# Kernel tuning notes

Hardware: AMD Instinct MI355X
Metric: run time of the kernel (lower is better)

Reference implementation:

```python
import jax, jax.numpy as jnp
import numpy as np
import math

DIM_MODEL = 1024
N_HEAD = 16
NUM_NEURON = 64
MAX_LEN = 2048
B, S = 4, 2048


def setup_inputs() -> dict:
    key = jax.random.key(0)
    ks = jax.random.split(key, 11)
    d, p = DIM_MODEL, N_HEAD * NUM_NEURON
    sc_in = 1.0 / math.sqrt(d)
    sc_p = 1.0 / math.sqrt(p)
    return {
        "q": jax.random.normal(ks[0], (B, S, d), jnp.float32),
        "k": jax.random.normal(ks[1], (B, S, d), jnp.float32),
        "v": jax.random.normal(ks[2], (B, S, d), jnp.float32),
        "Wq": jax.random.normal(ks[3], (d, p), jnp.float32) * sc_in,
        "bq": jnp.zeros((p,), jnp.float32),
        "Wk": jax.random.normal(ks[4], (d, p), jnp.float32) * sc_in,
        "bk": jnp.zeros((p,), jnp.float32),
        "Wv": jax.random.normal(ks[5], (d, p), jnp.float32) * sc_in,
        "bv": jnp.zeros((p,), jnp.float32),
        "Wf": jax.random.normal(ks[6], (p, d), jnp.float32) * sc_p,
        "bf": jnp.zeros((d,), jnp.float32),
    }


def _split_heads(x):  # [B,S,H*Dh] -> [B,H,S,Dh]
    b, s, _ = x.shape
    return x.reshape(b, s, N_HEAD, NUM_NEURON).transpose(0, 2, 1, 3)


def reference(q, k, v, Wq, bq, Wk, bk, Wv, bv, Wf, bf):
    qh = _split_heads(q @ Wq + bq)
    kh = _split_heads(k @ Wk + bk)
    vh = _split_heads(v @ Wv + bv)
    # NOTE: original scales by 1/sqrt(max_len), not 1/sqrt(head_dim)
    scores = jnp.einsum("bhqd,bhkd->bhqk", qh, kh) / math.sqrt(MAX_LEN)
    s = scores.shape[-1]
    causal = jnp.tril(jnp.ones((s, s), bool))  # [S,S]
    scores = jnp.where(causal[None, None], scores, -jnp.inf)
    attn = jax.nn.softmax(scores, axis=-1)
    out = jnp.einsum("bhqk,bhkd->bhqd", attn, vh)  # [B,H,S,Dh]
    c = out.transpose(0, 2, 1, 3).reshape(out.shape[0], out.shape[2], N_HEAD * NUM_NEURON)
    return c @ Wf + bf
```

## Files before the change

kernel.cpp:

```cpp
#include <hip/hip_runtime.h>
#include <stdint.h>

#define DMODEL 1024
#define NHEAD 16
#define DH 64
#define BB 4
#define SS 2048
#define MROWS (BB * SS)

typedef __bf16 bfx8 __attribute__((ext_vector_type(8)));
typedef float f32x4 __attribute__((ext_vector_type(4)));
typedef float fvec4 __attribute__((ext_vector_type(4)));
typedef int i32x4 __attribute__((ext_vector_type(4)));
typedef unsigned short u16x8 __attribute__((ext_vector_type(8)));
typedef unsigned short u16x4 __attribute__((ext_vector_type(4)));

__device__ __forceinline__ unsigned short f2bf(float f) {
    union { float f; unsigned int u; } v; v.f = f;
    unsigned int r = v.u + 0x7FFFu + ((v.u >> 16) & 1u);
    return (unsigned short)(r >> 16);
}

__device__ __forceinline__ unsigned int cvtpk(float lo, float hi) {
    unsigned int r;
    asm("v_cvt_pk_bf16_f32 %0, %1, %2" : "=v"(r) : "v"(lo), "v"(hi));
    return r;
}

typedef __attribute__((address_space(1))) const void gas_t;
typedef __attribute__((address_space(3))) void las_t;
__device__ __forceinline__ void gload_lds16(const void* g, void* l) {
    __builtin_amdgcn_global_load_lds((gas_t*)g, (las_t*)l, 16, 0, 0);
}

__device__ __forceinline__ int sigma_k(int i) {
    return (i & 0x20) | ((i & 0x0C) << 1) | ((i & 0x10) >> 2) | (i & 3);
}

__global__ void cvt3_kernel(const float* __restrict__ s0, const float* __restrict__ s1,
                            const float* __restrict__ s2,
                            unsigned short* __restrict__ d0, unsigned short* __restrict__ d1,
                            unsigned short* __restrict__ d2, int n8)
{
    const float* s = (blockIdx.y == 0) ? s0 : (blockIdx.y == 1) ? s1 : s2;
    unsigned short* d = (blockIdx.y == 0) ? d0 : (blockIdx.y == 1) ? d1 : d2;
    int i = blockIdx.x * blockDim.x + threadIdx.x;
    if (i >= n8) return;
    fvec4 a = *reinterpret_cast<const fvec4*>(&s[(size_t)i * 8]);
    fvec4 b = *reinterpret_cast<const fvec4*>(&s[(size_t)i * 8 + 4]);
    u16x8 o;
    #pragma unroll
    for (int j = 0; j < 4; ++j) { o[j] = f2bf(a[j]); o[j + 4] = f2bf(b[j]); }
    *reinterpret_cast<u16x8*>(&d[(size_t)i * 8]) = o;
}

__global__ void transpose_cvt3_kernel(const float* __restrict__ W0, unsigned short* __restrict__ T0,
                                      const float* __restrict__ W1, unsigned short* __restrict__ T1,
                                      const float* __restrict__ W2, unsigned short* __restrict__ T2)
{
    const float* W = (blockIdx.z == 0) ? W0 : (blockIdx.z == 1) ? W1 : W2;
    unsigned short* Wt = (blockIdx.z == 0) ? T0 : (blockIdx.z == 1) ? T1 : T2;
    __shared__ unsigned short t[64][72];
    const int tid = threadIdx.x;
    const int r0 = blockIdx.y * 64, c0 = blockIdx.x * 64;
    #pragma unroll
    for (int i = 0; i < 4; ++i) {
        int idx = tid + i * 256;
        int r = idx >> 4, c4 = idx & 15;
        fvec4 v = *reinterpret_cast<const fvec4*>(&W[(size_t)(r0 + r) * DMODEL + c0 + c4 * 4]);
        #pragma unroll
        for (int j = 0; j < 4; ++j) t[c4 * 4 + j][r] = f2bf(v[j]);
    }
    __syncthreads();
    #pragma unroll
    for (int i = 0; i < 2; ++i) {
        int idx = tid + i * 256;
        int r = idx >> 3, c8 = idx & 7;
        u16x8 v = *reinterpret_cast<const u16x8*>(&t[r][c8 * 8]);
        *reinterpret_cast<u16x8*>(&Wt[(size_t)(c0 + r) * DMODEL + r0 + c8 * 8]) = v;
    }
}

struct GArg {
    const unsigned short* A;
    const unsigned short* Bt;
    const float* bias;
    void* O;
    float osc;
    int mode;
};

__global__ __launch_bounds__(256, 2)
void gemm_kernel(GArg g0, GArg g1, int M, int N, int K)
{
    const GArg g = blockIdx.z ? g1 : g0;
    __shared__ unsigned short sA[128 * 64];
    __shared__ unsigned short sB[128 * 64];
    const int tid  = threadIdx.x;
    const int lane = tid & 63;
    const int wave = tid >> 6;
    const int wm = (wave >> 1) * 64, wn = (wave & 1) * 64;
    const int m0 = blockIdx.x * 128, n0 = blockIdx.y * 128;
    const int lr = lane & 15;
    const int lg = lane >> 4;

    f32x4 acc[4][4] = {};

    for (int kk0 = 0; kk0 < K; kk0 += 64) {
        __syncthreads();
        #pragma unroll
        for (int i = 0; i < 4; ++i) {
            int c = tid + i * 256;
            int row = c >> 3, col8 = c & 7;
            gload_lds16(&g.A[(size_t)(m0 + row) * K + kk0 + col8 * 8], &sA[c * 8]);
        }
        #pragma unroll
        for (int i = 0; i < 4; ++i) {
            int c = tid + i * 256;
            int row = c >> 3, col8 = c & 7;
            gload_lds16(&g.Bt[(size_t)(n0 + row) * K + kk0 + col8 * 8], &sB[c * 8]);
        }
        __syncthreads();

        bfx8 af[4][2], bfr[4][2];
        #pragma unroll
        for (int m = 0; m < 4; ++m)
            #pragma unroll
            for (int kk = 0; kk < 2; ++kk)
                af[m][kk] = *reinterpret_cast<const bfx8*>(
                    &sA[(wm + m * 16 + lr) * 64 + kk * 32 + lg * 8]);
        #pragma unroll
        for (int n = 0; n < 4; ++n)
            #pragma unroll
            for (int kk = 0; kk < 2; ++kk)
                bfr[n][kk] = *reinterpret_cast<const bfx8*>(
                    &sB[(wn + n * 16 + lr) * 64 + kk * 32 + lg * 8]);
        #pragma unroll
        for (int kk = 0; kk < 2; ++kk)
            #pragma unroll
            for (int m = 0; m < 4; ++m)
                #pragma unroll
                for (int n = 0; n < 4; ++n)
                    acc[m][n] = __builtin_amdgcn_mfma_f32_16x16x32_bf16(
                        af[m][kk], bfr[n][kk], acc[m][n], 0, 0, 0);
    }

    #pragma unroll
    for (int n = 0; n < 4; ++n) {
        int col = n0 + wn + n * 16 + lr;
        float bv = g.bias[col];
        #pragma unroll
        for (int m = 0; m < 4; ++m) {
            int rowb = m0 + wm + m * 16 + lg * 4;
            float val[4];
            #pragma unroll
            for (int r = 0; r < 4; ++r) val[r] = (acc[m][n][r] + bv) * g.osc;
            if (g.mode == 0) {
                #pragma unroll
                for (int r = 0; r < 4; ++r)
                    ((unsigned short*)g.O)[(size_t)(rowb + r) * N + col] = f2bf(val[r]);
            } else if (g.mode == 2) {
                #pragma unroll
                for (int r = 0; r < 4; ++r)
                    ((float*)g.O)[(size_t)(rowb + r) * N + col] = val[r];
            } else {
                int bq = rowb >> 11, s = rowb & 2047;
                int hh = col >> 6, d = col & 63;
                u16x4 pk;
                #pragma unroll
                for (int r = 0; r < 4; ++r) pk[r] = f2bf(val[r]);
                size_t idx = ((size_t)(bq * 16 + hh) * 64 + d) * 2048 + s;
                *reinterpret_cast<u16x4*>(&((unsigned short*)g.O)[idx]) = pk;
            }
        }
    }
}

__global__ __launch_bounds__(256, 2)
void attn_kernel(const unsigned short* __restrict__ Q,
                 const unsigned short* __restrict__ K,
                 const unsigned short* __restrict__ Vt,
                 unsigned short* __restrict__ C)
{
    __shared__ unsigned short sK[64 * 64];
    __shared__ unsigned short sV[64 * 64];

    const int tid  = threadIdx.x;
    const int lane = tid & 63;
    const int wave = tid >> 6;
    const int lr = lane & 15, lg = lane >> 4;
    const int bh = blockIdx.x;
    const int qt = (int)(gridDim.y - 1) - (int)blockIdx.y;
    const int b = bh >> 4, h = bh & 15;
    const int q0 = qt * 128;
    const size_t rowbase = (size_t)b * SS;
    const int hcol = h * DH;

    const int srow = tid >> 3, sc8 = tid & 7;
    const int sig0 = sigma_k(srow), sig1 = sigma_k(srow + 32);
    const int woff0 = srow * 64 + ((sc8 ^ (srow & 7)) * 8);
    const int woff1 = (srow + 32) * 64 + ((sc8 ^ (srow & 7)) * 8);
    const int p0 = lg ^ (lr & 7);

    bfx8 aq[2][2];
    #pragma unroll
    for (int m = 0; m < 2; ++m) {
        int qr = q0 + wave * 32 + m * 16 + lr;
        const unsigned short* p = &Q[(rowbase + qr) * DMODEL + hcol + lg * 8];
        aq[m][0] = *reinterpret_cast<const bfx8*>(p);
        aq[m][1] = *reinterpret_cast<const bfx8*>(p + 32);
    }

    float m_run[2] = {0.f, 0.f};
    f32x4 l4[2] = {};
    f32x4 acc_o[2][4] = {};
    bool mz = true;
    const int qmax_wave = q0 + wave * 32 + 31;
    const int ntiles = 2 * qt + 2;

    u16x8 rk0, rk1, rv0, rv1;
    {
        rk0 = *reinterpret_cast<const u16x8*>(&K[(rowbase + 0 + sig0) * DMODEL + hcol + sc8 * 8]);
        rk1 = *reinterpret_cast<const u16x8*>(&K[(rowbase + 0 + sig1) * DMODEL + hcol + sc8 * 8]);
        rv0 = *reinterpret_cast<const u16x8*>(&Vt[((size_t)bh * DH + srow) * SS + 0 + sc8 * 8]);
        rv1 = *reinterpret_cast<const u16x8*>(&Vt[((size_t)bh * DH + srow + 32) * SS + 0 + sc8 * 8]);
    }

    for (int t = 0; t < ntiles; ++t) {
        __syncthreads();
        *reinterpret_cast<u16x8*>(&sK[woff0]) = rk0;
        *reinterpret_cast<u16x8*>(&sK[woff1]) = rk1;
        *reinterpret_cast<u16x8*>(&sV[woff0]) = rv0;
        *reinterpret_cast<u16x8*>(&sV[woff1]) = rv1;
        __syncthreads();
        if (t + 1 < ntiles) {
            const int kk = (t + 1) * 64;
            rk0 = *reinterpret_cast<const u16x8*>(&K[(rowbase + kk + sig0) * DMODEL + hcol + sc8 * 8]);
            rk1 = *reinterpret_cast<const u16x8*>(&K[(rowbase + kk + sig1) * DMODEL + hcol + sc8 * 8]);
            rv0 = *reinterpret_cast<const u16x8*>(&Vt[((size_t)bh * DH + srow) * SS + kk + sc8 * 8]);
            rv1 = *reinterpret_cast<const u16x8*>(&Vt[((size_t)bh * DH + srow + 32) * SS + kk + sc8 * 8]);
        }
        const int k0 = t * 64;
        if (k0 > qmax_wave) continue;

        f32x4 sc[2][4];
        __builtin_amdgcn_s_setprio(1);
        #pragma unroll
        for (int nf = 0; nf < 4; ++nf) {
            int i = nf * 16 + lr;
            bfx8 ak0 = *reinterpret_cast<const bfx8*>(&sK[i * 64 + p0 * 8]);
            bfx8 ak1 = *reinterpret_cast<const bfx8*>(&sK[i * 64 + (p0 ^ 4) * 8]);
            #pragma unroll
            for (int m = 0; m < 2; ++m) {
                f32x4 s = {0.f, 0.f, 0.f, 0.f};
                s = __builtin_amdgcn_mfma_f32_16x16x32_bf16(ak0, aq[m][0], s, 0, 0, 0);
                s = __builtin_amdgcn_mfma_f32_16x16x32_bf16(ak1, aq[m][1], s, 0, 0, 0);
                sc[m][nf] = s;
            }
        }
        __builtin_amdgcn_s_setprio(0);
        #pragma unroll
        for (int m = 0; m < 2; ++m) {
            if (k0 + 63 > q0 + wave * 32 + m * 16) {
                int qrow = q0 + wave * 32 + m * 16 + lr;
                #pragma unroll
                for (int nf = 0; nf < 4; ++nf) {
                    int kb = k0 + ((nf >> 1) << 5) + (lg << 3) + ((nf & 1) << 2);
                    #pragma unroll
                    for (int r = 0; r < 4; ++r)
                        if (kb + r > qrow) sc[m][nf][r] = -3.0e38f;
                }
            }
        }
        f32x4 mx4 = sc[0][0];
        #pragma unroll
        for (int m = 0; m < 2; ++m)
            #pragma unroll
            for (int nf = 0; nf < 4; ++nf)
                #pragma unroll
                for (int r = 0; r < 4; ++r) mx4[r] = fmaxf(mx4[r], sc[m][nf][r]);
        float pmax = fmaxf(fmaxf(mx4[0], mx4[1]), fmaxf(mx4[2], mx4[3]));
        if (mz && __all(pmax <= 8.0f)) {
            #pragma unroll
            for (int m = 0; m < 2; ++m)
                #pragma unroll
                for (int nf = 0; nf < 4; ++nf) {
                    #pragma unroll
                    for (int r = 0; r < 4; ++r)
                        sc[m][nf][r] = __builtin_exp2f(sc[m][nf][r]);
                    l4[m] += sc[m][nf];
                }
        } else {
            mz = false;
            #pragma unroll
            for (int m = 0; m < 2; ++m) {
                float mx = -3.0e38f;
                #pragma unroll
                for (int nf = 0; nf < 4; ++nf)
                    #pragma unroll
                    for (int r = 0; r < 4; ++r) mx = fmaxf(mx, sc[m][nf][r]);
                mx = fmaxf(mx, __shfl_xor(mx, 16, 64));
                mx = fmaxf(mx, __shfl_xor(mx, 32, 64));
                float mnew = fmaxf(m_run[m], mx);
                float fs = __builtin_exp2f(m_run[m] - mnew);
                m_run[m] = mnew;
                f32x4 ps = {0.f, 0.f, 0.f, 0.f};
                #pragma unroll
                for (int nf = 0; nf < 4; ++nf) {
                    #pragma unroll
                    for (int r = 0; r < 4; ++r)
                        sc[m][nf][r] = __builtin_exp2f(sc[m][nf][r] - mnew);
                    ps += sc[m][nf];
                }
                #pragma unroll
                for (int r = 0; r < 4; ++r) l4[m][r] = l4[m][r] * fs + ps[r];
                #pragma unroll
                for (int r = 0; r < 4; ++r) {
                    float fsa = __shfl(fs, lg * 4 + r, 64);
                    #pragma unroll
                    for (int d = 0; d < 4; ++d) acc_o[m][d][r] *= fsa;
                }
            }
        }
        #pragma unroll
        for (int h2 = 0; h2 < 2; ++h2) {
            union { i32x4 i; bfx8 b; } pa[2];
            #pragma unroll
            for (int m = 0; m < 2; ++m) {
                pa[m].i[0] = cvtpk(sc[m][2 * h2][0],     sc[m][2 * h2][1]);
                pa[m].i[1] = cvtpk(sc[m][2 * h2][2],     sc[m][2 * h2][3]);
                pa[m].i[2] = cvtpk(sc[m][2 * h2 + 1][0], sc[m][2 * h2 + 1][1]);
                pa[m].i[3] = cvtpk(sc[m][2 * h2 + 1][2], sc[m][2 * h2 + 1][3]);
            }
            __builtin_amdgcn_s_setprio(1);
            #pragma unroll
            for (int d = 0; d < 4; ++d) {
                int i = d * 16 + lr;
                int pv = ((h2 << 2) | lg) ^ (lr & 7);
                bfx8 bv0 = *reinterpret_cast<const bfx8*>(&sV[i * 64 + pv * 8]);
                acc_o[0][d] = __builtin_amdgcn_mfma_f32_16x16x32_bf16(pa[0].b, bv0, acc_o[0][d], 0, 0, 0);
                acc_o[1][d] = __builtin_amdgcn_mfma_f32_16x16x32_bf16(pa[1].b, bv0, acc_o[1][d], 0, 0, 0);
            }
            __builtin_amdgcn_s_setprio(0);
        }
    }

    #pragma unroll
    for (int m = 0; m < 2; ++m) {
        float l = (l4[m][0] + l4[m][1]) + (l4[m][2] + l4[m][3]);
        l += __shfl_xor(l, 16, 64);
        l += __shfl_xor(l, 32, 64);
        float linv = 1.0f / l;
        float linva[4];
        #pragma unroll
        for (int r = 0; r < 4; ++r) linva[r] = __shfl(linv, lg * 4 + r, 64);
        const int qrb = q0 + wave * 32 + m * 16 + lg * 4;
        #pragma unroll
        for (int d = 0; d < 4; ++d) {
            int col = hcol + d * 16 + lr;
            #pragma unroll
            for (int r = 0; r < 4; ++r)
                C[(rowbase + qrb + r) * DMODEL + col] = f2bf(acc_o[m][d][r] * linva[r]);
        }
    }
}

extern "C" void kernel_launch(void* const* d_in, const int* in_sizes, int n_in,
                              void* d_out, int out_size, void* d_ws, size_t ws_size,
                              hipStream_t stream)
{
    const float* q  = (const float*)d_in[0];
    const float* k  = (const float*)d_in[1];
    const float* v  = (const float*)d_in[2];
    const float* Wq = (const float*)d_in[3];
    const float* bq = (const float*)d_in[4];
    const float* Wk = (const float*)d_in[5];
    const float* bk = (const float*)d_in[6];
    const float* Wv = (const float*)d_in[7];
    const float* bv = (const float*)d_in[8];
    const float* Wf = (const float*)d_in[9];
    const float* bf = (const float*)d_in[10];

    unsigned short* ws = (unsigned short*)d_ws;
    const size_t SZ = (size_t)MROWS * DMODEL;
    unsigned short* ws0 = ws;
    unsigned short* ws1 = ws + SZ;
    unsigned short* ws2 = ws + 2 * SZ;
    unsigned short* ws3 = ws + 3 * SZ;

    unsigned short* scr = (unsigned short*)d_out;
    unsigned short* WqT = scr;
    unsigned short* WkT = scr + 1048576;
    unsigned short* WvT = scr + 2097152;
    unsigned short* Qb  = scr + 4194304;

    const float qscale = 0.02209708691207961f * 1.44269504088896341f;

    const int n8 = (int)(SZ / 8);
    cvt3_kernel<<<dim3((n8 + 255) / 256, 3), 256, 0, stream>>>(q, k, v, ws0, ws1, ws2, n8);

    transpose_cvt3_kernel<<<dim3(16, 16, 3), 256, 0, stream>>>(Wq, WqT, Wk, WkT, Wv, WvT);

    {
        GArg gq{ws0, WqT, bq, Qb,  qscale, 0};
        GArg gk{ws1, WkT, bk, ws3, 1.0f,   0};
        gemm_kernel<<<dim3(64, 8, 2), 256, 0, stream>>>(gq, gk, MROWS, DMODEL, DMODEL);
    }
    {
        GArg gv{ws2, WvT, bv, ws0, 1.0f, 3};
        gemm_kernel<<<dim3(64, 8, 1), 256, 0, stream>>>(gv, gv, MROWS, DMODEL, DMODEL);
    }
    transpose_cvt3_kernel<<<dim3(16, 16, 1), 256, 0, stream>>>(Wf, ws2, Wf, ws2, Wf, ws2);

    attn_kernel<<<dim3(BB * NHEAD, SS / 128), 256, 0, stream>>>(Qb, ws3, ws0, ws1);

    {
        GArg gf{ws1, ws2, bf, (float*)d_out, 1.0f, 2};
        gemm_kernel<<<dim3(64, 8, 1), 256, 0, stream>>>(gf, gf, MROWS, DMODEL, DMODEL);
    }
}
```

Measured before the change: 213.6 us.

## Double-buffer K/V in LDS with smaller 64-row query tiles and remapped grid

Measured after the change: 267.7 us. 1.25x slower.

```diff
diff --git a/kernel.cpp b/kernel.cpp
--- a/kernel.cpp
+++ b/kernel.cpp
@@ -176,30 +176,36 @@
     }
 }
 
-__global__ __launch_bounds__(256, 2)
+__global__ __launch_bounds__(128, 4)
 void attn_kernel(const unsigned short* __restrict__ Q,
                  const unsigned short* __restrict__ K,
                  const unsigned short* __restrict__ Vt,
                  unsigned short* __restrict__ C)
 {
-    __shared__ unsigned short sK[64 * 64];
-    __shared__ unsigned short sV[64 * 64];
+    __shared__ unsigned short sK[2][4096];
+    __shared__ unsigned short sV[2][4096];
 
     const int tid  = threadIdx.x;
     const int lane = tid & 63;
     const int wave = tid >> 6;
     const int lr = lane & 15, lg = lane >> 4;
-    const int bh = blockIdx.x;
-    const int qt = (int)(gridDim.y - 1) - (int)blockIdx.y;
+    const int g  = blockIdx.x;
+    const int j  = g & 63;
+    const int bh = ((j & 7) << 3) | (j >> 3);
+    const int qt = 31 - (g >> 6);
     const int b = bh >> 4, h = bh & 15;
-    const int q0 = qt * 128;
+    const int q0 = qt * 64;
     const size_t rowbase = (size_t)b * SS;
     const int hcol = h * DH;
 
     const int srow = tid >> 3, sc8 = tid & 7;
-    const int sig0 = sigma_k(srow), sig1 = sigma_k(srow + 32);
-    const int woff0 = srow * 64 + ((sc8 ^ (srow & 7)) * 8);
-    const int woff1 = (srow + 32) * 64 + ((sc8 ^ (srow & 7)) * 8);
+    const int swz = (sc8 ^ (srow & 7)) * 8;
+    int sgrow[4], woff[4];
+    #pragma unroll
+    for (int i = 0; i < 4; ++i) {
+        sgrow[i] = sigma_k(srow + 16 * i);
+        woff[i]  = (srow + 16 * i) * 64 + swz;
+    }
     const int p0 = lg ^ (lr & 7);
 
     bfx8 aq[2][2];
@@ -215,41 +221,42 @@
     f32x4 l4[2] = {};
     f32x4 acc_o[2][4] = {};
     bool mz = true;
-    const int qmax_wave = q0 + wave * 32 + 31;
-    const int ntiles = 2 * qt + 2;
-
-    u16x8 rk0, rk1, rv0, rv1;
-    {
-        rk0 = *reinterpret_cast<const u16x8*>(&K[(rowbase + 0 + sig0) * DMODEL + hcol + sc8 * 8]);
-        rk1 = *reinterpret_cast<const u16x8*>(&K[(rowbase + 0 + sig1) * DMODEL + hcol + sc8 * 8]);
-        rv0 = *reinterpret_cast<const u16x8*>(&Vt[((size_t)bh * DH + srow) * SS + 0 + sc8 * 8]);
-        rv1 = *reinterpret_cast<const u16x8*>(&Vt[((size_t)bh * DH + srow + 32) * SS + 0 + sc8 * 8]);
-    }
+    const int ntiles = qt + 1;
+
+    u16x8 rk[4], rv[4];
+    #pragma unroll
+    for (int i = 0; i < 4; ++i) {
+        rk[i] = *reinterpret_cast<const u16x8*>(
+            &K[(rowbase + sgrow[i]) * DMODEL + hcol + sc8 * 8]);
+        rv[i] = *reinterpret_cast<const u16x8*>(
+            &Vt[((size_t)bh * DH + srow + 16 * i) * SS + sc8 * 8]);
+    }
+    #pragma unroll
+    for (int i = 0; i < 4; ++i) {
+        *reinterpret_cast<u16x8*>(&sK[0][woff[i]]) = rk[i];
+        *reinterpret_cast<u16x8*>(&sV[0][woff[i]]) = rv[i];
+    }
+    __syncthreads();
 
     for (int t = 0; t < ntiles; ++t) {
-        __syncthreads();
-        *reinterpret_cast<u16x8*>(&sK[woff0]) = rk0;
-        *reinterpret_cast<u16x8*>(&sK[woff1]) = rk1;
-        *reinterpret_cast<u16x8*>(&sV[woff0]) = rv0;
-        *reinterpret_cast<u16x8*>(&sV[woff1]) = rv1;
-        __syncthreads();
-        if (t + 1 < ntiles) {
-            const int kk = (t + 1) * 64;
-            rk0 = *reinterpret_cast<const u16x8*>(&K[(rowbase + kk + sig0) * DMODEL + hcol + sc8 * 8]);
-            rk1 = *reinterpret_cast<const u16x8*>(&K[(rowbase + kk + sig1) * DMODEL + hcol + sc8 * 8]);
-            rv0 = *reinterpret_cast<const u16x8*>(&Vt[((size_t)bh * DH + srow) * SS + kk + sc8 * 8]);
-            rv1 = *reinterpret_cast<const u16x8*>(&Vt[((size_t)bh * DH + srow + 32) * SS + kk + sc8 * 8]);
-        }
+        const int cur = t & 1, nxt = cur ^ 1;
         const int k0 = t * 64;
-        if (k0 > qmax_wave) continue;
+        const bool more = (t + 1 < ntiles);
+        if (more) {
+            const int kk = k0 + 64;
+            #pragma unroll
+            for (int i = 0; i < 4; ++i)
+                rk[i] = *reinterpret_cast<const u16x8*>(
+                    &K[(rowbase + kk + sgrow[i]) * DMODEL + hcol + sc8 * 8]);
+        }
 
         f32x4 sc[2][4];
         __builtin_amdgcn_s_setprio(1);
         #pragma unroll
         for (int nf = 0; nf < 4; ++nf) {
             int i = nf * 16 + lr;
-            bfx8 ak0 = *reinterpret_cast<const bfx8*>(&sK[i * 64 + p0 * 8]);
-            bfx8 ak1 = *reinterpret_cast<const bfx8*>(&sK[i * 64 + (p0 ^ 4) * 8]);
+            bfx8 ak0 = *reinterpret_cast<const bfx8*>(&sK[cur][i * 64 + p0 * 8]);
+            bfx8 ak1 = *reinterpret_cast<const bfx8*>(&sK[cur][i * 64 + (p0 ^ 4) * 8]);
             #pragma unroll
             for (int m = 0; m < 2; ++m) {
                 f32x4 s = {0.f, 0.f, 0.f, 0.f};
@@ -322,6 +329,13 @@
                 }
             }
         }
+        if (more) {
+            const int kk = k0 + 64;
+            #pragma unroll
+            for (int i = 0; i < 4; ++i)
+                rv[i] = *reinterpret_cast<const u16x8*>(
+                    &Vt[((size_t)bh * DH + srow + 16 * i) * SS + kk + sc8 * 8]);
+        }
         #pragma unroll
         for (int h2 = 0; h2 < 2; ++h2) {
             union { i32x4 i; bfx8 b; } pa[2];
@@ -337,12 +351,20 @@
             for (int d = 0; d < 4; ++d) {
                 int i = d * 16 + lr;
                 int pv = ((h2 << 2) | lg) ^ (lr & 7);
-                bfx8 bv0 = *reinterpret_cast<const bfx8*>(&sV[i * 64 + pv * 8]);
+                bfx8 bv0 = *reinterpret_cast<const bfx8*>(&sV[cur][i * 64 + pv * 8]);
                 acc_o[0][d] = __builtin_amdgcn_mfma_f32_16x16x32_bf16(pa[0].b, bv0, acc_o[0][d], 0, 0, 0);
                 acc_o[1][d] = __builtin_amdgcn_mfma_f32_16x16x32_bf16(pa[1].b, bv0, acc_o[1][d], 0, 0, 0);
             }
             __builtin_amdgcn_s_setprio(0);
         }
+        if (more) {
+            #pragma unroll
+            for (int i = 0; i < 4; ++i) {
+                *reinterpret_cast<u16x8*>(&sK[nxt][woff[i]]) = rk[i];
+                *reinterpret_cast<u16x8*>(&sV[nxt][woff[i]]) = rv[i];
+            }
+        }
+        __syncthreads();
     }
 
     #pragma unroll
@@ -412,7 +434,7 @@
     }
     transpose_cvt3_kernel<<<dim3(16, 16, 1), 256, 0, stream>>>(Wf, ws2, Wf, ws2, Wf, ws2);
 
-    attn_kernel<<<dim3(BB * NHEAD, SS / 128), 256, 0, stream>>>(Qb, ws3, ws0, ws1);
+    attn_kernel<<<dim3(2048), 128, 0, stream>>>(Qb, ws3, ws0, ws1);
 
     {
         GArg gf{ws1, ws2, bf, (float*)d_out, 1.0f, 2};
```

## Pair causal query tiles per block and use 8 waves of 16 rows

Applied to the files above, without the earlier changes.

After: 208.9 us. 2.2% less time.

```diff
diff --git a/kernel.cpp b/kernel.cpp
--- a/kernel.cpp
+++ b/kernel.cpp
@@ -176,191 +176,165 @@
     }
 }
 
-__global__ __launch_bounds__(256, 2)
+__global__ __launch_bounds__(512, 4)
 void attn_kernel(const unsigned short* __restrict__ Q,
                  const unsigned short* __restrict__ K,
                  const unsigned short* __restrict__ Vt,
                  unsigned short* __restrict__ C)
 {
-    __shared__ unsigned short sK[64 * 64];
-    __shared__ unsigned short sV[64 * 64];
+    __shared__ unsigned short sK[4096];
+    __shared__ unsigned short sV[4096];
 
     const int tid  = threadIdx.x;
     const int lane = tid & 63;
     const int wave = tid >> 6;
     const int lr = lane & 15, lg = lane >> 4;
     const int bh = blockIdx.x;
-    const int qt = (int)(gridDim.y - 1) - (int)blockIdx.y;
+    const int p  = blockIdx.y;
     const int b = bh >> 4, h = bh & 15;
-    const int q0 = qt * 128;
     const size_t rowbase = (size_t)b * SS;
     const int hcol = h * DH;
 
     const int srow = tid >> 3, sc8 = tid & 7;
-    const int sig0 = sigma_k(srow), sig1 = sigma_k(srow + 32);
-    const int woff0 = srow * 64 + ((sc8 ^ (srow & 7)) * 8);
-    const int woff1 = (srow + 32) * 64 + ((sc8 ^ (srow & 7)) * 8);
+    const int sig  = sigma_k(srow);
+    const int woff = srow * 64 + ((sc8 ^ (srow & 7)) * 8);
     const int p0 = lg ^ (lr & 7);
 
-    bfx8 aq[2][2];
-    #pragma unroll
-    for (int m = 0; m < 2; ++m) {
-        int qr = q0 + wave * 32 + m * 16 + lr;
-        const unsigned short* p = &Q[(rowbase + qr) * DMODEL + hcol + lg * 8];
-        aq[m][0] = *reinterpret_cast<const bfx8*>(p);
-        aq[m][1] = *reinterpret_cast<const bfx8*>(p + 32);
-    }
-
-    float m_run[2] = {0.f, 0.f};
-    f32x4 l4[2] = {};
-    f32x4 acc_o[2][4] = {};
-    bool mz = true;
-    const int qmax_wave = q0 + wave * 32 + 31;
-    const int ntiles = 2 * qt + 2;
-
-    u16x8 rk0, rk1, rv0, rv1;
-    {
-        rk0 = *reinterpret_cast<const u16x8*>(&K[(rowbase + 0 + sig0) * DMODEL + hcol + sc8 * 8]);
-        rk1 = *reinterpret_cast<const u16x8*>(&K[(rowbase + 0 + sig1) * DMODEL + hcol + sc8 * 8]);
-        rv0 = *reinterpret_cast<const u16x8*>(&Vt[((size_t)bh * DH + srow) * SS + 0 + sc8 * 8]);
-        rv1 = *reinterpret_cast<const u16x8*>(&Vt[((size_t)bh * DH + srow + 32) * SS + 0 + sc8 * 8]);
-    }
-
-    for (int t = 0; t < ntiles; ++t) {
-        __syncthreads();
-        *reinterpret_cast<u16x8*>(&sK[woff0]) = rk0;
-        *reinterpret_cast<u16x8*>(&sK[woff1]) = rk1;
-        *reinterpret_cast<u16x8*>(&sV[woff0]) = rv0;
-        *reinterpret_cast<u16x8*>(&sV[woff1]) = rv1;
-        __syncthreads();
-        if (t + 1 < ntiles) {
-            const int kk = (t + 1) * 64;
-            rk0 = *reinterpret_cast<const u16x8*>(&K[(rowbase + kk + sig0) * DMODEL + hcol + sc8 * 8]);
-            rk1 = *reinterpret_cast<const u16x8*>(&K[(rowbase + kk + sig1) * DMODEL + hcol + sc8 * 8]);
-            rv0 = *reinterpret_cast<const u16x8*>(&Vt[((size_t)bh * DH + srow) * SS + kk + sc8 * 8]);
-            rv1 = *reinterpret_cast<const u16x8*>(&Vt[((size_t)bh * DH + srow + 32) * SS + kk + sc8 * 8]);
-        }
-        const int k0 = t * 64;
-        if (k0 > qmax_wave) continue;
-
-        f32x4 sc[2][4];
-        __builtin_amdgcn_s_setprio(1);
-        #pragma unroll
-        for (int nf = 0; nf < 4; ++nf) {
-            int i = nf * 16 + lr;
-            bfx8 ak0 = *reinterpret_cast<const bfx8*>(&sK[i * 64 + p0 * 8]);
-            bfx8 ak1 = *reinterpret_cast<const bfx8*>(&sK[i * 64 + (p0 ^ 4) * 8]);
-            #pragma unroll
-            for (int m = 0; m < 2; ++m) {
+    #pragma unroll
+    for (int ph = 0; ph < 2; ++ph) {
+        const int qt = ph ? p : (15 - p);
+        const int q0 = qt * 128;
+
+        bfx8 aq[2];
+        {
+            int qr = q0 + wave * 16 + lr;
+            const unsigned short* qp = &Q[(rowbase + qr) * DMODEL + hcol + lg * 8];
+            aq[0] = *reinterpret_cast<const bfx8*>(qp);
+            aq[1] = *reinterpret_cast<const bfx8*>(qp + 32);
+        }
+
+        float m_run = 0.f;
+        f32x4 l4 = {};
+        f32x4 acc_o[4] = {};
+        bool mz = true;
+        const int qmax_wave = q0 + wave * 16 + 15;
+        const int ntiles = 2 * qt + 2;
+
+        u16x8 rk = *reinterpret_cast<const u16x8*>(
+            &K[(rowbase + sig) * DMODEL + hcol + sc8 * 8]);
+        u16x8 rv = *reinterpret_cast<const u16x8*>(
+            &Vt[((size_t)bh * DH + srow) * SS + sc8 * 8]);
+
+        for (int t = 0; t < ntiles; ++t) {
+            __syncthreads();
+            *reinterpret_cast<u16x8*>(&sK[woff]) = rk;
+            *reinterpret_cast<u16x8*>(&sV[woff]) = rv;
+            __syncthreads();
+            if (t + 1 < ntiles) {
+                const int kk = (t + 1) * 64;
+                rk = *reinterpret_cast<const u16x8*>(
+                    &K[(rowbase + kk + sig) * DMODEL + hcol + sc8 * 8]);
+                rv = *reinterpret_cast<const u16x8*>(
+                    &Vt[((size_t)bh * DH + srow) * SS + kk + sc8 * 8]);
+            }
+            const int k0 = t * 64;
+            if (k0 > qmax_wave) continue;
+
+            f32x4 sc[4];
+            __builtin_amdgcn_s_setprio(1);
+            #pragma unroll
+            for (int nf = 0; nf < 4; ++nf) {
+                int i = nf * 16 + lr;
+                bfx8 ak0 = *reinterpret_cast<const bfx8*>(&sK[i * 64 + p0 * 8]);
+                bfx8 ak1 = *reinterpret_cast<const bfx8*>(&sK[i * 64 + (p0 ^ 4) * 8]);
                 f32x4 s = {0.f, 0.f, 0.f, 0.f};
-                s = __builtin_amdgcn_mfma_f32_16x16x32_bf16(ak0, aq[m][0], s, 0, 0, 0);
-                s = __builtin_amdgcn_mfma_f32_16x16x32_bf16(ak1, aq[m][1], s, 0, 0, 0);
-                sc[m][nf] = s;
-            }
-        }
-        __builtin_amdgcn_s_setprio(0);
-        #pragma unroll
-        for (int m = 0; m < 2; ++m) {
-            if (k0 + 63 > q0 + wave * 32 + m * 16) {
-                int qrow = q0 + wave * 32 + m * 16 + lr;
+                s = __builtin_amdgcn_mfma_f32_16x16x32_bf16(ak0, aq[0], s, 0, 0, 0);
+                s = __builtin_amdgcn_mfma_f32_16x16x32_bf16(ak1, aq[1], s, 0, 0, 0);
+                sc[nf] = s;
+            }
+            __builtin_amdgcn_s_setprio(0);
+            if (k0 + 63 > q0 + wave * 16) {
+                int qrow = q0 + wave * 16 + lr;
                 #pragma unroll
                 for (int nf = 0; nf < 4; ++nf) {
                     int kb = k0 + ((nf >> 1) << 5) + (lg << 3) + ((nf & 1) << 2);
                     #pragma unroll
                     for (int r = 0; r < 4; ++r)
-                        if (kb + r > qrow) sc[m][nf][r] = -3.0e38f;
-                }
-            }
-        }
-        f32x4 mx4 = sc[0][0];
-        #pragma unroll
-        for (int m = 0; m < 2; ++m)
-            #pragma unroll
-            for (int nf = 0; nf < 4; ++nf)
-                #pragma unroll
-                for (int r = 0; r < 4; ++r) mx4[r] = fmaxf(mx4[r], sc[m][nf][r]);
-        float pmax = fmaxf(fmaxf(mx4[0], mx4[1]), fmaxf(mx4[2], mx4[3]));
-        if (mz && __all(pmax <= 8.0f)) {
-            #pragma unroll
-            for (int m = 0; m < 2; ++m)
+                        if (kb + r > qrow) sc[nf][r] = -3.0e38f;
+                }
+            }
+            f32x4 mx4 = sc[0];
+            #pragma unroll
+            for (int nf = 1; nf < 4; ++nf)
+                #pragma unroll
+                for (int r = 0; r < 4; ++r) mx4[r] = fmaxf(mx4[r], sc[nf][r]);
+            float pmax = fmaxf(fmaxf(mx4[0], mx4[1]), fmaxf(mx4[2], mx4[3]));
+            if (mz && __all(pmax <= 8.0f)) {
                 #pragma unroll
                 for (int nf = 0; nf < 4; ++nf) {
                     #pragma unroll
                     for (int r = 0; r < 4; ++r)
-                        sc[m][nf][r] = __builtin_exp2f(sc[m][nf][r]);
-                    l4[m] += sc[m][nf];
-                }
-        } else {
-            mz = false;
-            #pragma unroll
-            for (int m = 0; m < 2; ++m) {
-                float mx = -3.0e38f;
-                #pragma unroll
-                for (int nf = 0; nf < 4; ++nf)
-                    #pragma unroll
-                    for (int r = 0; r < 4; ++r) mx = fmaxf(mx, sc[m][nf][r]);
+                        sc[nf][r] = __builtin_exp2f(sc[nf][r]);
+                    l4 += sc[nf];
+                }
+            } else {
+                mz = false;
+                float mx = pmax;
                 mx = fmaxf(mx, __shfl_xor(mx, 16, 64));
                 mx = fmaxf(mx, __shfl_xor(mx, 32, 64));
-                float mnew = fmaxf(m_run[m], mx);
-                float fs = __builtin_exp2f(m_run[m] - mnew);
-                m_run[m] = mnew;
+                float mnew = fmaxf(m_run, mx);
+                float fs = __builtin_exp2f(m_run - mnew);
+                m_run = mnew;
                 f32x4 ps = {0.f, 0.f, 0.f, 0.f};
                 #pragma unroll
                 for (int nf = 0; nf < 4; ++nf) {
                     #pragma unroll
                     for (int r = 0; r < 4; ++r)
-                        sc[m][nf][r] = __builtin_exp2f(sc[m][nf][r] - mnew);
-                    ps += sc[m][nf];
-                }
-                #pragma unroll
-                for (int r = 0; r < 4; ++r) l4[m][r] = l4[m][r] * fs + ps[r];
+                        sc[nf][r] = __builtin_exp2f(sc[nf][r] - mnew);
+                    ps += sc[nf];
+                }
+                #pragma unroll
+                for (int r = 0; r < 4; ++r) l4[r] = l4[r] * fs + ps[r];
                 #pragma unroll
                 for (int r = 0; r < 4; ++r) {
                     float fsa = __shfl(fs, lg * 4 + r, 64);
                     #pragma unroll
-                    for (int d = 0; d < 4; ++d) acc_o[m][d][r] *= fsa;
-                }
-            }
-        }
-        #pragma unroll
-        for (int h2 = 0; h2 < 2; ++h2) {
-            union { i32x4 i; bfx8 b; } pa[2];
-            #pragma unroll
-            for (int m = 0; m < 2; ++m) {
-                pa[m].i[0] = cvtpk(sc[m][2 * h2][0],     sc[m][2 * h2][1]);
-                pa[m].i[1] = cvtpk(sc[m][2 * h2][2],     sc[m][2 * h2][3]);
-                pa[m].i[2] = cvtpk(sc[m][2 * h2 + 1][0], sc[m][2 * h2 + 1][1]);
-                pa[m].i[3] = cvtpk(sc[m][2 * h2 + 1][2], sc[m][2 * h2 + 1][3]);
-            }
-            __builtin_amdgcn_s_setprio(1);
-            #pragma unroll
-            for (int d = 0; d < 4; ++d) {
-                int i = d * 16 + lr;
-                int pv = ((h2 << 2) | lg) ^ (lr & 7);
-                bfx8 bv0 = *reinterpret_cast<const bfx8*>(&sV[i * 64 + pv * 8]);
-                acc_o[0][d] = __builtin_amdgcn_mfma_f32_16x16x32_bf16(pa[0].b, bv0, acc_o[0][d], 0, 0, 0);
-                acc_o[1][d] = __builtin_amdgcn_mfma_f32_16x16x32_bf16(pa[1].b, bv0, acc_o[1][d], 0, 0, 0);
-            }
-            __builtin_amdgcn_s_setprio(0);
-        }
-    }
-
-    #pragma unroll
-    for (int m = 0; m < 2; ++m) {
-        float l = (l4[m][0] + l4[m][1]) + (l4[m][2] + l4[m][3]);
+                    for (int d = 0; d < 4; ++d) acc_o[d][r] *= fsa;
+                }
+            }
+            #pragma unroll
+            for (int h2 = 0; h2 < 2; ++h2) {
+                union { i32x4 i; bfx8 b; } pa;
+                pa.i[0] = cvtpk(sc[2 * h2][0],     sc[2 * h2][1]);
+                pa.i[1] = cvtpk(sc[2 * h2][2],     sc[2 * h2][3]);
+                pa.i[2] = cvtpk(sc[2 * h2 + 1][0], sc[2 * h2 + 1][1]);
+                pa.i[3] = cvtpk(sc[2 * h2 + 1][2], sc[2 * h2 + 1][3]);
+                __builtin_amdgcn_s_setprio(1);
+                #pragma unroll
+                for (int d = 0; d < 4; ++d) {
+                    int i = d * 16 + lr;
+                    int pv = ((h2 << 2) | lg) ^ (lr & 7);
+                    bfx8 bv0 = *reinterpret_cast<const bfx8*>(&sV[i * 64 + pv * 8]);
+                    acc_o[d] = __builtin_amdgcn_mfma_f32_16x16x32_bf16(pa.b, bv0, acc_o[d], 0, 0, 0);
+                }
+                __builtin_amdgcn_s_setprio(0);
+            }
+        }
+
+        float l = (l4[0] + l4[1]) + (l4[2] + l4[3]);
         l += __shfl_xor(l, 16, 64);
         l += __shfl_xor(l, 32, 64);
         float linv = 1.0f / l;
         float linva[4];
         #pragma unroll
         for (int r = 0; r < 4; ++r) linva[r] = __shfl(linv, lg * 4 + r, 64);
-        const int qrb = q0 + wave * 32 + m * 16 + lg * 4;
+        const int qrb = q0 + wave * 16 + lg * 4;
         #pragma unroll
         for (int d = 0; d < 4; ++d) {
             int col = hcol + d * 16 + lr;
             #pragma unroll
             for (int r = 0; r < 4; ++r)
-                C[(rowbase + qrb + r) * DMODEL + col] = f2bf(acc_o[m][d][r] * linva[r]);
+                C[(rowbase + qrb + r) * DMODEL + col] = f2bf(acc_o[d][r] * linva[r]);
         }
     }
 }
@@ -412,7 +386,7 @@
     }
     transpose_cvt3_kernel<<<dim3(16, 16, 1), 256, 0, stream>>>(Wf, ws2, Wf, ws2, Wf, ws2);
 
-    attn_kernel<<<dim3(BB * NHEAD, SS / 128), 256, 0, stream>>>(Qb, ws3, ws0, ws1);
+    attn_kernel<<<dim3(BB * NHEAD, 8), 512, 0, stream>>>(Qb, ws3, ws0, ws1);
 
     {
         GArg gf{ws1, ws2, bf, (float*)d_out, 1.0f, 2};
```
